# Optimization experiments

Measured on AMD Instinct MI355X. Metric: run time of the kernel, lower is better.

Reference implementation:

```python
import jax, jax.numpy as jnp
import numpy as np

B, T, C, H, W, F = 4, 8, 64, 32, 32, 16
N = T * H * W  # 8192, must equal num_frames*size*size for ffnn1


def setup_inputs() -> dict:
    key = jax.random.key(0)
    ks = jax.random.split(key, 8)
    s = 1.0 / np.sqrt(C).astype(np.float32)
    sN = 1.0 / np.sqrt(N).astype(np.float32)
    return {
        "x": jax.random.normal(ks[0], (B, T, C, H, W), jnp.float32),
        "x1": jax.random.normal(ks[1], (B, T, C, H, W), jnp.float32),
        "conv1_w": jax.random.normal(ks[2], (F, C), jnp.float32) * s,
        "conv1_b": jax.random.normal(ks[3], (F,), jnp.float32) * 0.01,
        "g3_w": jax.random.normal(ks[4], (F, C), jnp.float32) * s,
        "g3_b": jax.random.normal(ks[5], (F,), jnp.float32) * 0.01,
        "ffnn1_w": jax.random.normal(ks[6], (N, N), jnp.float32) * sN,
        "ffnn1_b": jax.random.normal(ks[7], (N,), jnp.float32) * 0.01,
    }


def reference(x, x1, conv1_w, conv1_b, g3_w, g3_b, ffnn1_w, ffnn1_b):
    # x: [B,T,C,H,W]; x1 is accepted by the original forward but unused.
    b, t, c, h, w = x.shape
    nf = conv1_w.shape[0]
    # input.transpose(1,2).reshape(B, C, T*H*W)
    xr = x.transpose(0, 2, 1, 3, 4).reshape(b, c, t * h * w)  # [B,C,N]
    # Conv1d(C, F, 1) == pointwise linear over channels
    c1 = jnp.einsum('fc,bcn->bnf', conv1_w, xr) + conv1_b      # [B,N,F]
    # AvgPool1d(kernel=F) over feature axis of length F -> mean
    pooled = c1.mean(axis=-1)                                   # [B,N]
    # ffnn1 (Linear N->N) + sigmoid (act == 1 branch)
    v = jax.nn.sigmoid(pooled @ ffnn1_w.T + ffnn1_b)            # [B,N]
    # G3 conv1d
    g3 = jnp.einsum('fc,bcn->bnf', g3_w, xr) + g3_b             # [B,N,F]
    # diag_embed(v) @ g3  ==  row-scale by v (fused broadcast multiply)
    out = v[:, :, None] * g3                                    # [B,N,F]
    out = out.reshape(b, t, h, w, nf).transpose(0, 1, 4, 2, 3)  # [B,T,F,H,W]
    return out
```

## Files before the change

kernel.cpp:

```cpp
#include <hip/hip_runtime.h>
#include <hip/hip_bf16.h>


#define HW 1024
#define Cc 64
#define Ff 16
#define Nn 8192

typedef __hip_bfloat16 bf16;

__device__ __forceinline__ float bf2f(bf16 h) { return __bfloat162float(h); }

template <bool F32>
__device__ __forceinline__ float ld1(const void* p, int i) {
    if constexpr (F32) return ((const float*)p)[i];
    else               return bf2f(((const bf16*)p)[i]);
}

template <bool F32>
__device__ __forceinline__ void ld8(const void* p, size_t i, float* dst) {
    if constexpr (F32) {
        const float* q = (const float*)p + i;
        float4 a = *reinterpret_cast<const float4*>(q);
        float4 b = *reinterpret_cast<const float4*>(q + 4);
        dst[0] = a.x; dst[1] = a.y; dst[2] = a.z; dst[3] = a.w;
        dst[4] = b.x; dst[5] = b.y; dst[6] = b.z; dst[7] = b.w;
    } else {
        const bf16* q = (const bf16*)p + i;
        uint4 u = *reinterpret_cast<const uint4*>(q);
        dst[0] = __uint_as_float(u.x << 16);
        dst[1] = __uint_as_float(u.x & 0xffff0000u);
        dst[2] = __uint_as_float(u.y << 16);
        dst[3] = __uint_as_float(u.y & 0xffff0000u);
        dst[4] = __uint_as_float(u.z << 16);
        dst[5] = __uint_as_float(u.z & 0xffff0000u);
        dst[6] = __uint_as_float(u.w << 16);
        dst[7] = __uint_as_float(u.w & 0xffff0000u);
    }
}

template <bool F32>
__device__ __forceinline__ void pool_body(const void* __restrict__ x,
                                          const void* __restrict__ conv1_w,
                                          const void* __restrict__ conv1_b,
                                          float* __restrict__ pooled) {
    __shared__ float wbar[Cc];
    __shared__ float bbar;
    int tid = threadIdx.x;
    if (tid < Cc) {
        float s = 0.f;
        #pragma unroll
        for (int f = 0; f < Ff; ++f) s += ld1<F32>(conv1_w, f * Cc + tid);
        wbar[tid] = s * (1.f / 16.f);
    }
    if (tid == 64) {
        float s = 0.f;
        #pragma unroll
        for (int f = 0; f < Ff; ++f) s += ld1<F32>(conv1_b, f);
        bbar = s * (1.f / 16.f);
    }
    __syncthreads();

    int bt = blockIdx.x >> 3;
    int hw = ((blockIdx.x & 7) << 7) + tid;
    size_t base = (size_t)bt * Cc * HW + hw;
    float acc = 0.f;
    #pragma unroll
    for (int c = 0; c < Cc; ++c) acc += wbar[c] * ld1<F32>(x, base + c * HW);

    int b = bt >> 3, t = bt & 7;
    pooled[b * Nn + t * HW + hw] = acc + bbar;
}

__global__ void pool_kernel(const void* __restrict__ x,
                            const void* __restrict__ conv1_w,
                            const void* __restrict__ conv1_b,
                            float* __restrict__ pooled,
                            int* __restrict__ flag) {
    __shared__ int sflag;
    __shared__ int wcnt[2];
    int tid = threadIdx.x;
    const unsigned short* xs = (const unsigned short*)x;
    unsigned short u0 = xs[4 * tid], u1 = xs[4 * tid + 2];
    int e0 = (u0 >> 7) & 0xFF, e1 = (u1 >> 7) & 0xFF;
    int c = ((e0 >= 0x6F && e0 <= 0x83) ? 1 : 0)
          + ((e1 >= 0x6F && e1 <= 0x83) ? 1 : 0);
    #pragma unroll
    for (int off = 32; off > 0; off >>= 1) c += __shfl_down(c, off);
    if ((tid & 63) == 0) wcnt[tid >> 6] = c;
    __syncthreads();
    if (tid == 0) {
        int f = (wcnt[0] + wcnt[1] < 128) ? 1 : 0;
        sflag = f;
        flag[0] = f;
    }
    __syncthreads();
    if (sflag) pool_body<true>(x, conv1_w, conv1_b, pooled);
    else       pool_body<false>(x, conv1_w, conv1_b, pooled);
}

template <bool F32>
__device__ __forceinline__ void gemv_out_body(const void* __restrict__ w,
                                              const void* __restrict__ bias,
                                              const float* __restrict__ pooled,
                                              const void* __restrict__ x,
                                              const void* __restrict__ g3_w,
                                              const void* __restrict__ g3_b,
                                              void* __restrict__ out) {
    int tid = threadIdx.x;
    int k = tid * 8;
    int n0 = blockIdx.x * 8;
    int t   = blockIdx.x >> 7;
    int hw0 = (blockIdx.x & 127) * 8;

    float pl[4][8];
    #pragma unroll
    for (int b = 0; b < 4; ++b) {
        float4 p0 = *reinterpret_cast<const float4*>(pooled + b * Nn + k);
        float4 p1 = *reinterpret_cast<const float4*>(pooled + b * Nn + k + 4);
        pl[b][0] = p0.x; pl[b][1] = p0.y; pl[b][2] = p0.z; pl[b][3] = p0.w;
        pl[b][4] = p1.x; pl[b][5] = p1.y; pl[b][6] = p1.z; pl[b][7] = p1.w;
    }

    float acc[8][4];
    #pragma unroll
    for (int r = 0; r < 8; ++r) {
        float wv[8];
        ld8<F32>(w, (size_t)(n0 + r) * Nn + k, wv);
        #pragma unroll
        for (int b = 0; b < 4; ++b) {
            float s = 0.f;
            #pragma unroll
            for (int j = 0; j < 8; ++j) s = fmaf(wv[j], pl[b][j], s);
            acc[r][b] = s;
        }
    }

    #pragma unroll
    for (int r = 0; r < 8; ++r)
        #pragma unroll
        for (int b = 0; b < 4; ++b)
            #pragma unroll
            for (int off = 32; off > 0; off >>= 1)
                acc[r][b] += __shfl_down(acc[r][b], off);

    __shared__ float red[16][32];
    __shared__ float vsh[4][8];
    __shared__ float xsh[4][Cc][8];
    __shared__ float ws[Ff][Cc + 1];
    __shared__ float bs[Ff];

    int wave = tid >> 6, lane = tid & 63;
    if (lane == 0) {
        #pragma unroll
        for (int r = 0; r < 8; ++r)
            #pragma unroll
            for (int b = 0; b < 4; ++b)
                red[wave][r * 4 + b] = acc[r][b];
    }
    __syncthreads();

    if (tid < 32) {
        int r = tid >> 2, b = tid & 3;
        float s = 0.f;
        #pragma unroll
        for (int wv2 = 0; wv2 < 16; ++wv2) s += red[wv2][tid];
        s += ld1<F32>(bias, n0 + r);
        vsh[b][r] = 1.f / (1.f + __expf(-s));
    }
    if (tid < 256) {
        int b = tid >> 6, c = tid & 63;
        float tmp[8];
        ld8<F32>(x, ((size_t)(b * 8 + t) * Cc + c) * HW + hw0, tmp);
        #pragma unroll
        for (int i = 0; i < 8; ++i) xsh[b][c][i] = tmp[i];
    }
    {
        int f = tid >> 6, c = tid & 63;
        ws[f][c] = ld1<F32>(g3_w, tid);
    }
    if (tid < Ff) bs[tid] = ld1<F32>(g3_b, tid);
    __syncthreads();

    if (tid < 512) {
        int b = tid >> 7, f = (tid >> 3) & 15, i = tid & 7;
        float a2 = bs[f];
        #pragma unroll
        for (int c = 0; c < Cc; ++c) a2 = fmaf(ws[f][c], xsh[b][c][i], a2);
        float r = vsh[b][i] * a2;
        size_t oi = ((size_t)(b * 8 + t) * Ff + f) * HW + hw0 + i;
        if constexpr (F32) ((float*)out)[oi] = r;
        else               ((bf16*)out)[oi] = __float2bfloat16(r);
    }
}

__global__ __launch_bounds__(1024)
void gemv_out_kernel(const void* __restrict__ w,
                     const void* __restrict__ bias,
                     const float* __restrict__ pooled,
                     const void* __restrict__ x,
                     const void* __restrict__ g3_w,
                     const void* __restrict__ g3_b,
                     void* __restrict__ out,
                     const int* __restrict__ flag) {
    if (flag[0]) gemv_out_body<true>(w, bias, pooled, x, g3_w, g3_b, out);
    else         gemv_out_body<false>(w, bias, pooled, x, g3_w, g3_b, out);
}

extern "C" void kernel_launch(void* const* d_in, const int* in_sizes, int n_in,
                              void* d_out, int out_size, void* d_ws, size_t ws_size,
                              hipStream_t stream) {
    const void* x       = d_in[0];
    const void* conv1_w = d_in[2];
    const void* conv1_b = d_in[3];
    const void* g3_w    = d_in[4];
    const void* g3_b    = d_in[5];
    const void* ffnn1_w = d_in[6];
    const void* ffnn1_b = d_in[7];

    int*   flag   = (int*)d_ws;
    float* pooled = (float*)d_ws + 16;

    pool_kernel<<<256, 128, 0, stream>>>(x, conv1_w, conv1_b, pooled, flag);
    gemv_out_kernel<<<1024, 1024, 0, stream>>>(ffnn1_w, ffnn1_b, pooled,
                                               x, g3_w, g3_b, d_out, flag);
}
```

Baseline: 400.7 us.

## Restructure fused GEMV to 256-thread blocks with per-wave rows and nontemporal weight loads

The fused GEMV+G3 kernel now runs 256 threads per block. Each wave owns two weight rows and loops over K, and its partial sums are reduced with shuffle-xor, so the cross-wave shared-memory reduction is gone. Weight loads use nontemporal hints so the streaming 256MB matrix does not pollute the cache. The G3 stage is vectorized with a transposed padded shared layout. The change is meant to raise occupancy and memory-level parallelism for the bandwidth-bound weight stream, at the cost of re-reading pooled from L2 per iteration.

```diff
diff --git a/kernel.cpp b/kernel.cpp
--- a/kernel.cpp
+++ b/kernel.cpp
@@ -8,6 +8,8 @@
 #define Nn 8192
 
 typedef __hip_bfloat16 bf16;
+typedef float vf4 __attribute__((ext_vector_type(4)));
+typedef unsigned int vu4 __attribute__((ext_vector_type(4)));
 
 __device__ __forceinline__ float bf2f(bf16 h) { return __bfloat162float(h); }
 
@@ -40,6 +42,28 @@
 }
 
 template <bool F32>
+__device__ __forceinline__ void ld8nt(const void* p, size_t i, float* dst) {
+    if constexpr (F32) {
+        const vf4* q = (const vf4*)((const float*)p + i);
+        vf4 a = __builtin_nontemporal_load(q);
+        vf4 b = __builtin_nontemporal_load(q + 1);
+        dst[0] = a[0]; dst[1] = a[1]; dst[2] = a[2]; dst[3] = a[3];
+        dst[4] = b[0]; dst[5] = b[1]; dst[6] = b[2]; dst[7] = b[3];
+    } else {
+        const vu4* q = (const vu4*)((const bf16*)p + i);
+        vu4 u = __builtin_nontemporal_load(q);
+        dst[0] = __uint_as_float(u[0] << 16);
+        dst[1] = __uint_as_float(u[0] & 0xffff0000u);
+        dst[2] = __uint_as_float(u[1] << 16);
+        dst[3] = __uint_as_float(u[1] & 0xffff0000u);
+        dst[4] = __uint_as_float(u[2] << 16);
+        dst[5] = __uint_as_float(u[2] & 0xffff0000u);
+        dst[6] = __uint_as_float(u[3] << 16);
+        dst[7] = __uint_as_float(u[3] & 0xffff0000u);
+    }
+}
+
+template <bool F32>
 __device__ __forceinline__ void pool_body(const void* __restrict__ x,
                                           const void* __restrict__ conv1_w,
                                           const void* __restrict__ conv1_b,
@@ -107,94 +131,108 @@
                                               const void* __restrict__ g3_w,
                                               const void* __restrict__ g3_b,
                                               void* __restrict__ out) {
-    int tid = threadIdx.x;
-    int k = tid * 8;
-    int n0 = blockIdx.x * 8;
-    int t   = blockIdx.x >> 7;
-    int hw0 = (blockIdx.x & 127) * 8;
-
-    float pl[4][8];
-    #pragma unroll
-    for (int b = 0; b < 4; ++b) {
-        float4 p0 = *reinterpret_cast<const float4*>(pooled + b * Nn + k);
-        float4 p1 = *reinterpret_cast<const float4*>(pooled + b * Nn + k + 4);
-        pl[b][0] = p0.x; pl[b][1] = p0.y; pl[b][2] = p0.z; pl[b][3] = p0.w;
-        pl[b][4] = p1.x; pl[b][5] = p1.y; pl[b][6] = p1.z; pl[b][7] = p1.w;
-    }
-
-    float acc[8][4];
-    #pragma unroll
-    for (int r = 0; r < 8; ++r) {
-        float wv[8];
-        ld8<F32>(w, (size_t)(n0 + r) * Nn + k, wv);
-        #pragma unroll
-        for (int b = 0; b < 4; ++b) {
-            float s = 0.f;
-            #pragma unroll
-            for (int j = 0; j < 8; ++j) s = fmaf(wv[j], pl[b][j], s);
-            acc[r][b] = s;
-        }
-    }
-
-    #pragma unroll
-    for (int r = 0; r < 8; ++r)
-        #pragma unroll
-        for (int b = 0; b < 4; ++b)
-            #pragma unroll
-            for (int off = 32; off > 0; off >>= 1)
-                acc[r][b] += __shfl_down(acc[r][b], off);
-
-    __shared__ float red[16][32];
+    int tid  = threadIdx.x;
+    int wave = tid >> 6, lane = tid & 63;
+    int n0   = blockIdx.x * 8;
+    int t    = blockIdx.x >> 7;
+    int hw0  = (blockIdx.x & 127) * 8;
+
+    __shared__ __align__(16) float xsh[4][8][68];
+    __shared__ __align__(16) float g3s[Ff][68];
     __shared__ float vsh[4][8];
-    __shared__ float xsh[4][Cc][8];
-    __shared__ float ws[Ff][Cc + 1];
-    __shared__ float bs[Ff];
-
-    int wave = tid >> 6, lane = tid & 63;
-    if (lane == 0) {
-        #pragma unroll
-        for (int r = 0; r < 8; ++r)
-            #pragma unroll
-            for (int b = 0; b < 4; ++b)
-                red[wave][r * 4 + b] = acc[r][b];
-    }
-    __syncthreads();
-
-    if (tid < 32) {
-        int r = tid >> 2, b = tid & 3;
-        float s = 0.f;
-        #pragma unroll
-        for (int wv2 = 0; wv2 < 16; ++wv2) s += red[wv2][tid];
-        s += ld1<F32>(bias, n0 + r);
-        vsh[b][r] = 1.f / (1.f + __expf(-s));
-    }
-    if (tid < 256) {
+    __shared__ float bsh[Ff];
+
+    {
         int b = tid >> 6, c = tid & 63;
         float tmp[8];
         ld8<F32>(x, ((size_t)(b * 8 + t) * Cc + c) * HW + hw0, tmp);
         #pragma unroll
-        for (int i = 0; i < 8; ++i) xsh[b][c][i] = tmp[i];
-    }
+        for (int i = 0; i < 8; ++i) xsh[b][i][c] = tmp[i];
+    }
+    #pragma unroll
+    for (int rep = 0; rep < 4; ++rep) {
+        int idx = rep * 256 + tid;
+        g3s[idx >> 6][idx & 63] = ld1<F32>(g3_w, idx);
+    }
+    if (tid < Ff) bsh[tid] = ld1<F32>(g3_b, tid);
+
+    int r0 = n0 + wave * 2;
+    float acc[2][4];
+    #pragma unroll
+    for (int r = 0; r < 2; ++r)
+        #pragma unroll
+        for (int b = 0; b < 4; ++b) acc[r][b] = 0.f;
+
+    #pragma unroll 2
+    for (int it = 0; it < 16; ++it) {
+        int k = it * 512 + lane * 8;
+        float wv0[8], wv1[8];
+        ld8nt<F32>(w, (size_t)r0 * Nn + k, wv0);
+        ld8nt<F32>(w, (size_t)(r0 + 1) * Nn + k, wv1);
+        #pragma unroll
+        for (int b = 0; b < 4; ++b) {
+            const float* pp = pooled + b * Nn + k;
+            vf4 p0 = *(const vf4*)pp;
+            vf4 p1 = *(const vf4*)(pp + 4);
+            float pv[8] = {p0[0], p0[1], p0[2], p0[3],
+                           p1[0], p1[1], p1[2], p1[3]};
+            #pragma unroll
+            for (int j = 0; j < 8; ++j) {
+                acc[0][b] = fmaf(wv0[j], pv[j], acc[0][b]);
+                acc[1][b] = fmaf(wv1[j], pv[j], acc[1][b]);
+            }
+        }
+    }
+
+    #pragma unroll
+    for (int r = 0; r < 2; ++r)
+        #pragma unroll
+        for (int b = 0; b < 4; ++b) {
+            float s = acc[r][b];
+            #pragma unroll
+            for (int off = 1; off < 64; off <<= 1) s += __shfl_xor(s, off);
+            acc[r][b] = s;
+        }
+
+    if (lane == 0) {
+        #pragma unroll
+        for (int r = 0; r < 2; ++r) {
+            float bb = ld1<F32>(bias, r0 + r);
+            #pragma unroll
+            for (int b = 0; b < 4; ++b)
+                vsh[b][wave * 2 + r] = 1.f / (1.f + __expf(-(acc[r][b] + bb)));
+        }
+    }
+    __syncthreads();
+
     {
-        int f = tid >> 6, c = tid & 63;
-        ws[f][c] = ld1<F32>(g3_w, tid);
-    }
-    if (tid < Ff) bs[tid] = ld1<F32>(g3_b, tid);
-    __syncthreads();
-
-    if (tid < 512) {
-        int b = tid >> 7, f = (tid >> 3) & 15, i = tid & 7;
-        float a2 = bs[f];
-        #pragma unroll
-        for (int c = 0; c < Cc; ++c) a2 = fmaf(ws[f][c], xsh[b][c][i], a2);
-        float r = vsh[b][i] * a2;
-        size_t oi = ((size_t)(b * 8 + t) * Ff + f) * HW + hw0 + i;
-        if constexpr (F32) ((float*)out)[oi] = r;
-        else               ((bf16*)out)[oi] = __float2bfloat16(r);
-    }
-}
-
-__global__ __launch_bounds__(1024)
+        int b = tid >> 6, f = (tid >> 2) & 15, i0 = (tid & 3) * 2;
+        float a0 = bsh[f], a1 = a0;
+        #pragma unroll
+        for (int c4 = 0; c4 < Cc; c4 += 4) {
+            vf4 gv = *(const vf4*)&g3s[f][c4];
+            vf4 x0 = *(const vf4*)&xsh[b][i0][c4];
+            vf4 x1 = *(const vf4*)&xsh[b][i0 + 1][c4];
+            #pragma unroll
+            for (int j = 0; j < 4; ++j) {
+                a0 = fmaf(gv[j], x0[j], a0);
+                a1 = fmaf(gv[j], x1[j], a1);
+            }
+        }
+        float v0 = vsh[b][i0] * a0;
+        float v1 = vsh[b][i0 + 1] * a1;
+        size_t oi = ((size_t)(b * 8 + t) * Ff + f) * HW + hw0 + i0;
+        if constexpr (F32) {
+            *reinterpret_cast<float2*>((float*)out + oi) = make_float2(v0, v1);
+        } else {
+            __hip_bfloat162 hh = __halves2bfloat162(__float2bfloat16(v0),
+                                                    __float2bfloat16(v1));
+            *reinterpret_cast<__hip_bfloat162*>((bf16*)out + oi) = hh;
+        }
+    }
+}
+
+__global__ __launch_bounds__(256, 4)
 void gemv_out_kernel(const void* __restrict__ w,
                      const void* __restrict__ bias,
                      const float* __restrict__ pooled,
@@ -222,6 +260,6 @@
     float* pooled = (float*)d_ws + 16;
 
     pool_kernel<<<256, 128, 0, stream>>>(x, conv1_w, conv1_b, pooled, flag);
-    gemv_out_kernel<<<1024, 1024, 0, stream>>>(ffnn1_w, ffnn1_b, pooled,
-                                               x, g3_w, g3_b, d_out, flag);
-}
+    gemv_out_kernel<<<1024, 256, 0, stream>>>(ffnn1_w, ffnn1_b, pooled,
+                                              x, g3_w, g3_b, d_out, flag);
+}
```

Result: no change. 397.9 us (-0.7%).
